# Performance work log

Measured on AMD Instinct MI355X. Metric: run time of the kernel, lower is better.

## Reference

```python
import jax, jax.numpy as jnp
import numpy as np

N_HEAD = 8
HEAD_DIM = 64
DIM = 512
INNER = N_HEAD * HEAD_DIM
ATT_THRESHOLD = 1e-4
SCALE = HEAD_DIM ** -0.5


def setup_inputs() -> dict:
    key = jax.random.key(0)
    ks = jax.random.split(key, 7)
    b, n, dn = 2, 2048, 2048
    fr = jax.random.normal(ks[0], (b, n, DIM), dtype=jnp.float32)
    dt = jax.random.normal(ks[1], (b, dn, DIM), dtype=jnp.float32)
    s = DIM ** -0.5
    Wq = jax.random.normal(ks[2], (DIM, INNER), dtype=jnp.float32) * s
    Wk = jax.random.normal(ks[3], (DIM, INNER), dtype=jnp.float32) * s
    Wv = jax.random.normal(ks[4], (DIM, INNER), dtype=jnp.float32) * s
    Wo = jax.random.normal(ks[5], (INNER, DIM), dtype=jnp.float32) * (INNER ** -0.5)
    bo = jax.random.normal(ks[6], (DIM,), dtype=jnp.float32) * 0.01
    return {"fr": fr, "dt": dt, "Wq": Wq, "Wk": Wk, "Wv": Wv, "Wo": Wo, "bo": bo}


def reference(fr, dt, Wq, Wk, Wv, Wo, bo):
    b, n, _ = fr.shape
    dn = dt.shape[1]
    # projections -> [b, seq, n_head, head_dim]
    q = (fr @ Wq).reshape(b, n, N_HEAD, HEAD_DIM)
    k = (dt @ Wk).reshape(b, dn, N_HEAD, HEAD_DIM)
    v = (dt @ Wv).reshape(b, dn, N_HEAD, HEAD_DIM)
    # full attention matrix [b, h, n, dn]
    scores = jnp.einsum('bihd,bjhd->bhij', q, k) * SCALE
    attn = jax.nn.softmax(scores, axis=-1)
    # torch .clip(t) with one positional arg clamps the MIN: max(attn, t)
    attn = jnp.maximum(attn, ATT_THRESHOLD) - ATT_THRESHOLD
    attn = attn / jnp.sum(attn, axis=-1, keepdims=True)
    out = jnp.einsum('bhij,bjhd->bihd', attn, v).reshape(b, n, INNER)
    return out @ Wo + bo
```

## Files before the change

kernel.cpp:

```cpp
#include <hip/hip_runtime.h>
#include <hip/hip_bf16.h>

#define BB 2
#define SEQ 2048
#define NHEAD 8
#define HD 64
#define ATT_T 1e-4f
#define QSCALE 0.18033688011112042f

typedef short s16x8 __attribute__((ext_vector_type(8)));
typedef float f32x16 __attribute__((ext_vector_type(16)));

#define MFMA32(a, b, c) __builtin_amdgcn_mfma_f32_32x32x16_bf16((a), (b), (c), 0, 0, 0)
#define EXP2(x) __builtin_amdgcn_exp2f(x)
#define SB0() __builtin_amdgcn_sched_barrier(0)
#define WAITVM0() __builtin_amdgcn_s_waitcnt(0x0F70)
#define WAITVM4() __builtin_amdgcn_s_waitcnt(0x0F74)
#define WAITVM8() __builtin_amdgcn_s_waitcnt(0x0F78)
#define WAITVM12() __builtin_amdgcn_s_waitcnt(0x0F7C)

__device__ __forceinline__ unsigned short bfr(float x) {
  __hip_bfloat16 h = __float2bfloat16(x);
  return __builtin_bit_cast(unsigned short, h);
}
__device__ __forceinline__ unsigned int packbf(float a, float b) {
  return (unsigned int)bfr(a) | ((unsigned int)bfr(b) << 16);
}
__device__ __forceinline__ unsigned int permpack(float a, float b) {
  return __builtin_amdgcn_perm(__builtin_bit_cast(unsigned int, b),
                               __builtin_bit_cast(unsigned int, a), 0x07060302u);
}
__device__ __forceinline__ void async16(const void* g, void* l) {
  __builtin_amdgcn_global_load_lds(
      (const __attribute__((address_space(1))) unsigned int*)g,
      (__attribute__((address_space(3))) unsigned int*)l, 16, 0, 0);
}
__device__ __forceinline__ void plswap(unsigned a, unsigned b, int lh,
                                       unsigned& x, unsigned& z) {
#if __has_builtin(__builtin_amdgcn_permlane32_swap)
  typedef unsigned uint2v __attribute__((ext_vector_type(2)));
  uint2v r = __builtin_amdgcn_permlane32_swap(a, b, false, false);
  x = r[0];
  z = r[1];
#else
  unsigned ea = (unsigned)__shfl_xor((int)a, 32);
  unsigned eb = (unsigned)__shfl_xor((int)b, 32);
  x = lh ? eb : a;
  z = lh ? b : ea;
#endif
}


__global__ __launch_bounds__(256) void prep(const float* __restrict__ fr,
                                            const float* __restrict__ dt,
                                            const float* __restrict__ w0,
                                            const float* __restrict__ w1,
                                            const float* __restrict__ w2,
                                            const float* __restrict__ w3,
                                            unsigned short* __restrict__ frB,
                                            unsigned short* __restrict__ dtB,
                                            unsigned short* __restrict__ o0,
                                            unsigned short* __restrict__ o1,
                                            unsigned short* __restrict__ o2,
                                            unsigned short* __restrict__ o3) {
  const int bid = blockIdx.x;
  if (bid < 2048) {
    const float* src = (bid < 1024) ? fr : dt;
    unsigned short* dst = (bid < 1024) ? frB : dtB;
    const int chunk = (bid < 1024) ? bid : bid - 1024;
    const size_t base = (size_t)chunk * 2048 + threadIdx.x * 8;
    float4 a = *(const float4*)(src + base);
    float4 b = *(const float4*)(src + base + 4);
    uint4 o;
    o.x = packbf(a.x, a.y);
    o.y = packbf(a.z, a.w);
    o.z = packbf(b.x, b.y);
    o.w = packbf(b.z, b.w);
    *(uint4*)(dst + base) = o;
    return;
  }
  __shared__ float tle[64][65];
  const int t = bid - 2048;
  const int z = t >> 6, by = (t >> 3) & 7, bx = t & 7;
  const float* W = z == 0 ? w0 : z == 1 ? w1 : z == 2 ? w2 : w3;
  unsigned short* WT = z == 0 ? o0 : z == 1 ? o1 : z == 2 ? o2 : o3;
  const int r0 = by * 64, c0 = bx * 64;
  const int tr = threadIdx.x >> 4;
  const int tc = threadIdx.x & 15;
  #pragma unroll
  for (int i = 0; i < 4; i++) {
    int r = tr + i * 16;
    float4 v = *(const float4*)(W + (size_t)(r0 + r) * 512 + c0 + tc * 4);
    tle[r][tc * 4 + 0] = v.x;
    tle[r][tc * 4 + 1] = v.y;
    tle[r][tc * 4 + 2] = v.z;
    tle[r][tc * 4 + 3] = v.w;
  }
  __syncthreads();
  #pragma unroll
  for (int i = 0; i < 4; i++) {
    int c = tr + i * 16;
    int rr = tc * 4;
    uint2 p;
    p.x = packbf(tle[rr + 0][c], tle[rr + 1][c]);
    p.y = packbf(tle[rr + 2][c], tle[rr + 3][c]);
    *(uint2*)(WT + (size_t)(c0 + c) * 512 + r0 + rr) = p;
  }
}

__global__ __launch_bounds__(256) void gemm_qkv(const unsigned short* __restrict__ frB,
                                                const unsigned short* __restrict__ dtB,
                                                const unsigned short* __restrict__ WqT,
                                                const unsigned short* __restrict__ WkT,
                                                const unsigned short* __restrict__ WvT,
                                                unsigned short* __restrict__ Qp,
                                                unsigned short* __restrict__ Kp,
                                                unsigned short* __restrict__ VTp) {
  __shared__ __align__(16) unsigned short smem[24576];
  unsigned short* Asm = smem;
  unsigned short* Bsm = smem + 8192;
  const int tid = threadIdx.x, lane = tid & 63, w = tid >> 6;
  const int l31 = lane & 31, lh = lane >> 5;
  const int m0 = blockIdx.y * 64, n0 = blockIdx.x * 128;
  const int z = blockIdx.z;
  const unsigned short* Ab = z == 0 ? frB : dtB;
  const unsigned short* BT = z == 0 ? WqT : (z == 1 ? WkT : WvT);
  unsigned short* OP = z == 0 ? Qp : (z == 1 ? Kp : VTp);
  const float scale = z == 0 ? QSCALE : 1.0f;

  const int rl = lane >> 3;
  const int cl8 = ((lane & 7) ^ rl) * 8;
  const int x7 = l31 & 7;

  auto stage = [&](int kt, int buf) {
    const int k0 = kt * 64;
    #pragma unroll
    for (int i = 0; i < 2; i++) {
      int s = w * 2 + i;
      async16(Ab + (size_t)(m0 + s * 8 + rl) * 512 + k0 + cl8,
              Asm + buf * 4096 + s * 512);
    }
    #pragma unroll
    for (int i = 0; i < 4; i++) {
      int s = w * 4 + i;
      async16(BT + (size_t)(n0 + s * 8 + rl) * 512 + k0 + cl8,
              Bsm + buf * 8192 + s * 512);
    }
  };

  f32x16 acc[2];
  #pragma unroll
  for (int j = 0; j < 2; j++)
    #pragma unroll
    for (int r = 0; r < 16; r++) acc[j][r] = 0.f;

  stage(0, 0);
  for (int kt = 0; kt < 8; ++kt) {
    __syncthreads();
    if (kt + 1 < 8) stage(kt + 1, (kt + 1) & 1);
    const int buf = kt & 1;
    const unsigned short* as = Asm + buf * 4096 + ((w & 1) * 32 + l31) * 64;
    const unsigned short* bs = Bsm + buf * 8192 + ((w >> 1) * 64 + l31) * 64;
    #pragma unroll
    for (int ks = 0; ks < 4; ++ks) {
      const int co = ((ks * 2 + lh) ^ x7) * 8;
      s16x8 af = *(const s16x8*)(as + co);
      s16x8 b0 = *(const s16x8*)(bs + co);
      s16x8 b1 = *(const s16x8*)(bs + 2048 + co);
      acc[0] = MFMA32(af, b0, acc[0]);
      acc[1] = MFMA32(af, b1, acc[1]);
    }
  }

  const int wm = (w & 1) * 32, wn = (w >> 1) * 64;
  const int bb = m0 >> 11, s0 = m0 & 2047;
  const int h0 = n0 >> 6, cbase = s0 >> 5;
  __syncthreads();
  if (z <= 1) {
    #pragma unroll
    for (int j = 0; j < 2; j++)
      #pragma unroll
      for (int r = 0; r < 16; r++) {
        int mm = wm + (r & 3) + 8 * (r >> 2) + 4 * lh;
        int nn = wn + j * 32 + l31;
        smem[mm * 136 + nn] = bfr(acc[j][r] * scale);
      }
    __syncthreads();
    #pragma unroll
    for (int it = 0; it < 4; ++it) {
      int u = tid + it * 256;
      int b = u >> 8, v = u & 255;
      int hp = b >> 1, cp = b & 1;
      int mm = cp * 32 + (v & 31);
      int nn = hp * 64 + ((v >> 6) << 4) + (((v >> 5) & 1) << 3);
      uint4 vdat = *(const uint4*)(smem + mm * 136 + nn);
      *(uint4*)(OP + ((size_t)(bb * NHEAD + h0 + hp)) * SEQ * HD +
                (size_t)(cbase + cp) * 2048 + v * 8) = vdat;
    }
  } else {
    #pragma unroll
    for (int j = 0; j < 2; j++)
      #pragma unroll
      for (int r = 0; r < 16; r += 2) {
        int mm = wm + (r & 3) + 8 * (r >> 2) + 4 * lh;
        int nn = wn + j * 32 + l31;
        *(unsigned int*)(smem + nn * 72 + mm) = packbf(acc[j][r], acc[j][r + 1]);
      }
    __syncthreads();
    #pragma unroll
    for (int it = 0; it < 4; ++it) {
      int u = tid + it * 256;
      int hp = u >> 9;
      int rem = u & 511;
      int cp = rem >> 8, v = rem & 255;
      int nn = hp * 64 + ((v >> 7) << 5) + (v & 31);
      int mm0 = cp * 32 + (((v >> 6) & 1) << 4) + (((v >> 5) & 1) << 3);
      uint4 vdat = *(const uint4*)(smem + nn * 72 + mm0);
      *(uint4*)(OP + ((size_t)(bb * NHEAD + h0 + hp)) * SEQ * HD +
                (size_t)(cbase + cp) * 2048 + v * 8) = vdat;
    }
  }
}

__global__ __launch_bounds__(256) void gemm_out(const unsigned short* __restrict__ A,
                                                const unsigned short* __restrict__ BT,
                                                const float* __restrict__ bias,
                                                float* __restrict__ O) {
  __shared__ __align__(16) unsigned short smem[16384];
  unsigned short* Asm = smem;
  unsigned short* Bsm = smem + 8192;
  const int tid = threadIdx.x, lane = tid & 63, w = tid >> 6;
  const int l31 = lane & 31, lh = lane >> 5;
  const int m0 = blockIdx.y * 64, n0 = blockIdx.x * 64;

  const int rl = lane >> 3;
  const int cl8 = ((lane & 7) ^ rl) * 8;
  const int x7 = l31 & 7;

  auto stage = [&](int kt, int buf) {
    const int k0 = kt * 64;
    #pragma unroll
    for (int i = 0; i < 2; i++) {
      int s = w * 2 + i;
      async16(A + (size_t)(m0 + s * 8 + rl) * 512 + k0 + cl8,
              Asm + buf * 4096 + s * 512);
      async16(BT + (size_t)(n0 + s * 8 + rl) * 512 + k0 + cl8,
              Bsm + buf * 4096 + s * 512);
    }
  };

  f32x16 acc;
  #pragma unroll
  for (int r = 0; r < 16; r++) acc[r] = 0.f;

  stage(0, 0);
  for (int kt = 0; kt < 8; ++kt) {
    __syncthreads();
    if (kt + 1 < 8) stage(kt + 1, (kt + 1) & 1);
    const int buf = kt & 1;
    const unsigned short* as = Asm + buf * 4096 + ((w & 1) * 32 + l31) * 64;
    const unsigned short* bs = Bsm + buf * 4096 + ((w >> 1) * 32 + l31) * 64;
    #pragma unroll
    for (int ks = 0; ks < 4; ++ks) {
      const int co = ((ks * 2 + lh) ^ x7) * 8;
      s16x8 af = *(const s16x8*)(as + co);
      s16x8 bf = *(const s16x8*)(bs + co);
      acc = MFMA32(af, bf, acc);
    }
  }

  const int wm = (w & 1) * 32, wn = (w >> 1) * 32;
  float bv = bias[n0 + wn + l31];
  #pragma unroll
  for (int r = 0; r < 16; r++) {
    int mm = wm + (r & 3) + 8 * (r >> 2) + 4 * lh;
    O[(size_t)(m0 + mm) * 512 + n0 + wn + l31] = acc[r] + bv;
  }
}

__global__ __launch_bounds__(256, 2) void attn_mfma(const unsigned short* __restrict__ Q,
                                                    const unsigned short* __restrict__ K,
                                                    const unsigned short* __restrict__ VT,
                                                    unsigned short* __restrict__ O) {
  __shared__ __align__(16) unsigned short arena[4][8192];
  __shared__ float larr[4][64];
  __shared__ float warr[4][64];

  const int tid = threadIdx.x;
  const int lane = tid & 63;
  const int w = tid >> 6;
  const int l31 = lane & 31, lh = lane >> 5;

  const int bid = blockIdx.x;
  const int g = bid & 7, j = bid >> 3;
  const int bh = g * 2 + (j >> 5);
  const int qt = j & 31;

  const unsigned short* Qh = Q + (size_t)bh * SEQ * HD;
  const unsigned short* Kh = K + (size_t)bh * SEQ * HD;
  const unsigned short* VTh = VT + (size_t)bh * SEQ * HD;

  s16x8 qf[2][4];
  #pragma unroll
  for (int q2 = 0; q2 < 2; q2++)
    #pragma unroll
    for (int t = 0; t < 4; t++)
      qf[q2][t] = *(const s16x8*)(Qh + (size_t)(qt * 2 + q2) * 2048 + t * 512 + lane * 8);

  unsigned short* kbuf = &arena[w][0];

  auto stageK = [&](int c, int slot) {
    const unsigned short* G = Kh + (size_t)(w * 16 + c) * 2048 + lane * 8;
    #pragma unroll
    for (int tt = 0; tt < 4; tt++)
      async16(G + tt * 512, kbuf + slot * 2048 + tt * 512);
  };

  f32x16 scp[2];
  auto qkt = [&](int slot) {
    s16x8 kf[4];
    #pragma unroll
    for (int tt = 0; tt < 4; tt++)
      kf[tt] = *(const s16x8*)(kbuf + slot * 2048 + tt * 512 + lane * 8);
    #pragma unroll
    for (int q2 = 0; q2 < 2; q2++) {
      f32x16 sc;
      #pragma unroll
      for (int r = 0; r < 16; r++) sc[r] = 0.f;
      #pragma unroll
      for (int tt = 0; tt < 4; tt++) sc = MFMA32(kf[tt], qf[q2][tt], sc);
      scp[q2] = sc;
    }
  };

  float lsum[2] = {0.f, 0.f};
  auto accum_l = [&]() {
    #pragma unroll
    for (int q2 = 0; q2 < 2; q2++) {
      float s0 = 0.f, s1 = 0.f, s2 = 0.f, s3 = 0.f;
      #pragma unroll
      for (int r = 0; r < 4; r++) {
        s0 += EXP2(scp[q2][r]);
        s1 += EXP2(scp[q2][4 + r]);
        s2 += EXP2(scp[q2][8 + r]);
        s3 += EXP2(scp[q2][12 + r]);
      }
      lsum[q2] += (s0 + s1) + (s2 + s3);
    }
  };

  stageK(0, 0);
  stageK(1, 1);
  stageK(2, 2);
  for (int c = 0; c < 16; ++c) {
    if (c + 3 < 16) stageK(c + 3, (c + 3) & 3);
    if (c > 0) accum_l();
    if (c < 13) { WAITVM12(); }
    else if (c == 13) { WAITVM8(); }
    else if (c == 14) { WAITVM4(); }
    else { WAITVM0(); }
    SB0();
    qkt(c & 3);
  }
  accum_l();
  #pragma unroll
  for (int q2 = 0; q2 < 2; q2++) lsum[q2] += __shfl_xor(lsum[q2], 32);
  if (lh == 0) { larr[w][l31] = lsum[0]; larr[w][32 + l31] = lsum[1]; }
  __syncthreads();
  float tl[2];
  #pragma unroll
  for (int q2 = 0; q2 < 2; q2++)
    tl[q2] = ATT_T * (larr[0][q2 * 32 + l31] + larr[1][q2 * 32 + l31] +
                      larr[2][q2 * 32 + l31] + larr[3][q2 * 32 + l31]);

  f32x16 acc[2][2];
  #pragma unroll
  for (int q2 = 0; q2 < 2; q2++)
    #pragma unroll
    for (int dh = 0; dh < 2; dh++)
      #pragma unroll
      for (int r = 0; r < 16; r++) acc[q2][dh][r] = 0.f;
  float wacc[2] = {0.f, 0.f};
  s16x8 vrA[4], vrB[4];

  auto loadV = [&](int c, s16x8(&vr)[4]) {
    const unsigned short* G = VTh + (size_t)(w * 16 + c) * 2048 + lane * 8;
    #pragma unroll
    for (int jj = 0; jj < 4; jj++)
      vr[jj] = *(const s16x8*)(G + jj * 512);
  };
  auto softmax_pv = [&](const s16x8(&vr)[4]) {
    s16x8 pf[2][2];
    #pragma unroll
    for (int q2 = 0; q2 < 2; q2++) {
      uint2 quads[4];
      #pragma unroll
      for (int gq = 0; gq < 4; gq++) {
        float u0 = fmaxf(EXP2(scp[q2][4 * gq + 0]) - tl[q2], 0.f);
        float u1 = fmaxf(EXP2(scp[q2][4 * gq + 1]) - tl[q2], 0.f);
        float u2 = fmaxf(EXP2(scp[q2][4 * gq + 2]) - tl[q2], 0.f);
        float u3 = fmaxf(EXP2(scp[q2][4 * gq + 3]) - tl[q2], 0.f);
        wacc[q2] += (u0 + u1) + (u2 + u3);
        quads[gq].x = permpack(u0, u1);
        quads[gq].y = permpack(u2, u3);
      }
      #pragma unroll
      for (int tp = 0; tp < 2; tp++) {
        unsigned x0, z0, x1, z1;
        plswap(quads[2 * tp].x, quads[2 * tp + 1].x, lh, x0, z0);
        plswap(quads[2 * tp].y, quads[2 * tp + 1].y, lh, x1, z1);
        uint4 fr;
        fr.x = x0; fr.y = x1; fr.z = z0; fr.w = z1;
        pf[q2][tp] = __builtin_bit_cast(s16x8, fr);
      }
    }
    #pragma unroll
    for (int q2 = 0; q2 < 2; q2++)
      #pragma unroll
      for (int dh = 0; dh < 2; dh++) {
        acc[q2][dh] = MFMA32(pf[q2][0], vr[dh * 2 + 0], acc[q2][dh]);
        acc[q2][dh] = MFMA32(pf[q2][1], vr[dh * 2 + 1], acc[q2][dh]);
      }
  };

  stageK(0, 0);
  stageK(1, 1);
  stageK(2, 2);
  loadV(0, vrA);
  for (int cc = 0; cc < 16; cc += 2) {
    if (cc > 0) {
      if (cc < 14) { WAITVM12(); } else { WAITVM8(); }
      SB0();
      softmax_pv(vrB);
    }
    loadV(cc + 1, vrB);
    if (cc + 3 < 16) stageK(cc + 3, (cc + 3) & 3);
    if (cc == 0) { WAITVM12(); }
    SB0();
    qkt(cc & 3);
    if (cc == 0) { WAITVM8(); }
    else if (cc < 14) { WAITVM12(); }
    else { WAITVM4(); }
    SB0();
    softmax_pv(vrA);
    if (cc + 2 < 16) loadV(cc + 2, vrA);
    if (cc + 4 < 16) stageK(cc + 4, (cc + 4) & 3);
    SB0();
    qkt((cc + 1) & 3);
  }
  WAITVM0();
  SB0();
  softmax_pv(vrB);

  #pragma unroll
  for (int q2 = 0; q2 < 2; q2++) wacc[q2] += __shfl_xor(wacc[q2], 32);
  if (lh == 0) { warr[w][l31] = wacc[0]; warr[w][32 + l31] = wacc[1]; }
  __syncthreads();

  float* plane0 = (float*)&arena[0][0];
  float* plane1 = (float*)&arena[1][0];

  if (w >= 2) {
    float* pl = (w == 2) ? plane0 : plane1;
    #pragma unroll
    for (int q2 = 0; q2 < 2; q2++)
      #pragma unroll
      for (int dh = 0; dh < 2; dh++)
        #pragma unroll
        for (int r = 0; r < 16; r++) {
          int ql = q2 * 32 + (r & 3) + 8 * (r >> 2) + 4 * lh;
          pl[ql * 64 + dh * 32 + l31] = acc[q2][dh][r];
        }
  }
  __syncthreads();
  if (w < 2) {
    float* pl = (w == 0) ? plane0 : plane1;
    #pragma unroll
    for (int q2 = 0; q2 < 2; q2++)
      #pragma unroll
      for (int dh = 0; dh < 2; dh++)
        #pragma unroll
        for (int r = 0; r < 16; r++) {
          int ql = q2 * 32 + (r & 3) + 8 * (r >> 2) + 4 * lh;
          acc[q2][dh][r] += pl[ql * 64 + dh * 32 + l31];
        }
  }
  __syncthreads();
  if (w == 1) {
    #pragma unroll
    for (int q2 = 0; q2 < 2; q2++)
      #pragma unroll
      for (int dh = 0; dh < 2; dh++)
        #pragma unroll
        for (int r = 0; r < 16; r++) {
          int ql = q2 * 32 + (r & 3) + 8 * (r >> 2) + 4 * lh;
          plane0[ql * 64 + dh * 32 + l31] = acc[q2][dh][r];
        }
  }
  __syncthreads();
  unsigned short* otile = &arena[2][0];
  if (w == 0) {
    #pragma unroll
    for (int q2 = 0; q2 < 2; q2++)
      #pragma unroll
      for (int dh = 0; dh < 2; dh++)
        #pragma unroll
        for (int r = 0; r < 16; r++) {
          int ql = q2 * 32 + (r & 3) + 8 * (r >> 2) + 4 * lh;
          float wt = warr[0][ql] + warr[1][ql] + warr[2][ql] + warr[3][ql];
          float v = (acc[q2][dh][r] + plane0[ql * 64 + dh * 32 + l31]) / wt;
          otile[ql * 64 + dh * 32 + l31] = bfr(v);
        }
  }
  __syncthreads();
  const int b = bh >> 3, h = bh & 7;
  #pragma unroll
  for (int it = 0; it < 2; ++it) {
    int c2 = tid + it * 256;
    int mm = c2 >> 3, seg = c2 & 7;
    uint4 vdat = *(const uint4*)(otile + mm * 64 + seg * 8);
    *(uint4*)(O + ((size_t)(b * SEQ + qt * 64 + mm)) * 512 + h * HD + seg * 8) = vdat;
  }
}

extern "C" void kernel_launch(void* const* d_in, const int* in_sizes, int n_in,
                              void* d_out, int out_size, void* d_ws, size_t ws_size,
                              hipStream_t stream) {
  const float* fr = (const float*)d_in[0];
  const float* dt = (const float*)d_in[1];
  const float* Wq = (const float*)d_in[2];
  const float* Wk = (const float*)d_in[3];
  const float* Wv = (const float*)d_in[4];
  const float* Wo = (const float*)d_in[5];
  const float* bo = (const float*)d_in[6];
  float* out = (float*)d_out;

  const size_t planeE = (size_t)BB * SEQ * 512;
  const size_t wE = 512 * 512;
  unsigned short* p = (unsigned short*)d_ws;
  unsigned short* WqT = p; p += wE;
  unsigned short* WkT = p; p += wE;
  unsigned short* WvT = p; p += wE;
  unsigned short* WoT = p; p += wE;
  unsigned short* Qp  = p; p += planeE;
  unsigned short* Kp  = p; p += planeE;
  unsigned short* VTp = p; p += planeE;
  unsigned short* aoB = p; p += planeE;

  unsigned short* frB = (unsigned short*)d_out;
  unsigned short* dtB = (unsigned short*)d_out + planeE;

  prep<<<2304, 256, 0, stream>>>(fr, dt, Wq, Wk, Wv, Wo, frB, dtB, WqT, WkT, WvT, WoT);

  gemm_qkv<<<dim3(4, 64, 3), 256, 0, stream>>>(frB, dtB, WqT, WkT, WvT, Qp, Kp, VTp);

  attn_mfma<<<BB * NHEAD * 32, 256, 0, stream>>>(Qp, Kp, VTp, aoB);

  gemm_out<<<dim3(8, 64), 256, 0, stream>>>(aoB, WoT, bo, out);
}
```

Baseline: 137.9 us.

## Double-buffer score registers to overlap QK^T MFMA with softmax-PV of previous chunk

```diff
diff --git a/kernel.cpp b/kernel.cpp
--- a/kernel.cpp
+++ b/kernel.cpp
@@ -15,9 +15,9 @@
 #define EXP2(x) __builtin_amdgcn_exp2f(x)
 #define SB0() __builtin_amdgcn_sched_barrier(0)
 #define WAITVM0() __builtin_amdgcn_s_waitcnt(0x0F70)
-#define WAITVM4() __builtin_amdgcn_s_waitcnt(0x0F74)
 #define WAITVM8() __builtin_amdgcn_s_waitcnt(0x0F78)
 #define WAITVM12() __builtin_amdgcn_s_waitcnt(0x0F7C)
+#define WAITVM16() __builtin_amdgcn_s_waitcnt(0x4F70)
 
 __device__ __forceinline__ unsigned short bfr(float x) {
   __hip_bfloat16 h = __float2bfloat16(x);
@@ -316,23 +316,23 @@
       async16(G + tt * 512, kbuf + slot * 2048 + tt * 512);
   };
 
-  f32x16 scp[2];
-  auto qkt = [&](int slot) {
+  auto qkt2 = [&](int slot, f32x16 (&sc)[2]) {
     s16x8 kf[4];
     #pragma unroll
     for (int tt = 0; tt < 4; tt++)
       kf[tt] = *(const s16x8*)(kbuf + slot * 2048 + tt * 512 + lane * 8);
     #pragma unroll
     for (int q2 = 0; q2 < 2; q2++) {
-      f32x16 sc;
-      #pragma unroll
-      for (int r = 0; r < 16; r++) sc[r] = 0.f;
-      #pragma unroll
-      for (int tt = 0; tt < 4; tt++) sc = MFMA32(kf[tt], qf[q2][tt], sc);
-      scp[q2] = sc;
-    }
-  };
-
+      f32x16 s;
+      #pragma unroll
+      for (int r = 0; r < 16; r++) s[r] = 0.f;
+      #pragma unroll
+      for (int tt = 0; tt < 4; tt++) s = MFMA32(kf[tt], qf[q2][tt], s);
+      sc[q2] = s;
+    }
+  };
+
+  f32x16 scp[2];
   float lsum[2] = {0.f, 0.f};
   auto accum_l = [&]() {
     #pragma unroll
@@ -357,10 +357,10 @@
     if (c > 0) accum_l();
     if (c < 13) { WAITVM12(); }
     else if (c == 13) { WAITVM8(); }
-    else if (c == 14) { WAITVM4(); }
+    else if (c == 14) { __builtin_amdgcn_s_waitcnt(0x0F74); }
     else { WAITVM0(); }
     SB0();
-    qkt(c & 3);
+    qkt2(c & 3, scp);
   }
   accum_l();
   #pragma unroll
@@ -382,6 +382,7 @@
       for (int r = 0; r < 16; r++) acc[q2][dh][r] = 0.f;
   float wacc[2] = {0.f, 0.f};
   s16x8 vrA[4], vrB[4];
+  f32x16 scpE[2], scpO[2];
 
   auto loadV = [&](int c, s16x8(&vr)[4]) {
     const unsigned short* G = VTh + (size_t)(w * 16 + c) * 2048 + lane * 8;
@@ -389,17 +390,17 @@
     for (int jj = 0; jj < 4; jj++)
       vr[jj] = *(const s16x8*)(G + jj * 512);
   };
-  auto softmax_pv = [&](const s16x8(&vr)[4]) {
+  auto softmax_pv = [&](const f32x16 (&sc)[2], const s16x8(&vr)[4]) {
     s16x8 pf[2][2];
     #pragma unroll
     for (int q2 = 0; q2 < 2; q2++) {
       uint2 quads[4];
       #pragma unroll
       for (int gq = 0; gq < 4; gq++) {
-        float u0 = fmaxf(EXP2(scp[q2][4 * gq + 0]) - tl[q2], 0.f);
-        float u1 = fmaxf(EXP2(scp[q2][4 * gq + 1]) - tl[q2], 0.f);
-        float u2 = fmaxf(EXP2(scp[q2][4 * gq + 2]) - tl[q2], 0.f);
-        float u3 = fmaxf(EXP2(scp[q2][4 * gq + 3]) - tl[q2], 0.f);
+        float u0 = fmaxf(EXP2(sc[q2][4 * gq + 0]) - tl[q2], 0.f);
+        float u1 = fmaxf(EXP2(sc[q2][4 * gq + 1]) - tl[q2], 0.f);
+        float u2 = fmaxf(EXP2(sc[q2][4 * gq + 2]) - tl[q2], 0.f);
+        float u3 = fmaxf(EXP2(sc[q2][4 * gq + 3]) - tl[q2], 0.f);
         wacc[q2] += (u0 + u1) + (u2 + u3);
         quads[gq].x = permpack(u0, u1);
         quads[gq].y = permpack(u2, u3);
@@ -427,30 +428,32 @@
   stageK(1, 1);
   stageK(2, 2);
   loadV(0, vrA);
-  for (int cc = 0; cc < 16; cc += 2) {
-    if (cc > 0) {
-      if (cc < 14) { WAITVM12(); } else { WAITVM8(); }
-      SB0();
-      softmax_pv(vrB);
-    }
+  WAITVM12();
+  SB0();
+  qkt2(0, scpE);
+  stageK(3, 3);
+  loadV(1, vrB);
+  WAITVM16();
+  SB0();
+  qkt2(1, scpO);
+  softmax_pv(scpE, vrA);
+  stageK(4, 0);
+  loadV(2, vrA);
+  for (int cc = 2; cc < 16; cc += 2) {
+    if (cc < 14) { WAITVM16(); } else { WAITVM12(); }
+    SB0();
+    qkt2(cc & 3, scpE);
+    softmax_pv(scpO, vrB);
+    if (cc + 3 < 16) stageK(cc + 3, (cc + 3) & 3);
     loadV(cc + 1, vrB);
-    if (cc + 3 < 16) stageK(cc + 3, (cc + 3) & 3);
-    if (cc == 0) { WAITVM12(); }
+    if (cc < 14) { WAITVM16(); } else { WAITVM8(); }
     SB0();
-    qkt(cc & 3);
-    if (cc == 0) { WAITVM8(); }
-    else if (cc < 14) { WAITVM12(); }
-    else { WAITVM4(); }
-    SB0();
-    softmax_pv(vrA);
+    qkt2((cc + 1) & 3, scpO);
+    softmax_pv(scpE, vrA);
+    if (cc + 4 < 16) stageK(cc + 4, (cc + 4) & 3);
     if (cc + 2 < 16) loadV(cc + 2, vrA);
-    if (cc + 4 < 16) stageK(cc + 4, (cc + 4) & 3);
-    SB0();
-    qkt((cc + 1) & 3);
-  }
-  WAITVM0();
-  SB0();
-  softmax_pv(vrB);
+  }
+  softmax_pv(scpO, vrB);
 
   #pragma unroll
   for (int q2 = 0; q2 < 2; q2++) wacc[q2] += __shfl_xor(wacc[q2], 32);
```

Result: slower. 143.5 us (+4.1%).
